# Performance work log

Hardware: AMD Instinct MI355X
Metric: run time of the kernel (lower is better)

## Reference

```python
import jax, jax.numpy as jnp
import numpy as np

N_NODES = 50000
N_EDGES = 800000
D_IN = 128
D_OUT = 128


def setup_inputs() -> dict:
    key = jax.random.key(0)
    k1, k2, k3, k4, k5 = jax.random.split(key, 5)
    x = jax.random.normal(k1, (N_NODES, D_IN), dtype=jnp.float32)
    edge_index = jax.random.randint(k2, (2, N_EDGES), 0, N_NODES, dtype=jnp.int64)
    scale = 1.0 / np.sqrt(D_IN)
    W_rel = jax.random.normal(k3, (D_OUT, D_IN), dtype=jnp.float32) * scale
    b_rel = jax.random.normal(k4, (D_OUT,), dtype=jnp.float32) * scale
    W_root = jax.random.normal(k5, (D_OUT, D_IN), dtype=jnp.float32) * scale
    return {"x": x, "edge_index": edge_index, "W_rel": W_rel, "b_rel": b_rel, "W_root": W_root}


def reference(x, edge_index, W_rel, b_rel, W_root):
    # PyG GraphConv (aggr='add'):
    #   out_i = W_rel @ (sum_{j->i} x_j) + b_rel + W_root @ x_i
    # followed by ReLU (normalization=None, dropout=0 -> identity).
    src = edge_index[0]  # message source j
    dst = edge_index[1]  # message target i
    n = x.shape[0]
    agg = jax.ops.segment_sum(x[src], dst, num_segments=n)  # [N, D_IN]
    out = agg @ W_rel.T + b_rel + x @ W_root.T              # [N, D_OUT]
    return jax.nn.relu(out)
```

## Files before the change

kernel.cpp:

```cpp
#include <hip/hip_runtime.h>
#include <hip/hip_bf16.h>


#define N_NODES 50000
#define N_EDGES 800000
#define D 128
#define SLOTS 40
#define NB 782
#define BCAP 1536
#define BINB 196
#define NPB 32
#define KC 32
#define SROW 136

#define CVT_N  (N_NODES * (D / 2))
#define PACK_N (8 * 8 * 64 * 8)

typedef __attribute__((ext_vector_type(8))) short short8;
typedef __attribute__((ext_vector_type(4))) float floatx4;

__device__ __forceinline__ float bf2f(unsigned short u) {
    return __uint_as_float((unsigned int)u << 16);
}
__device__ __forceinline__ unsigned short f2bf(float f) {
    __hip_bfloat16 h = __float2bfloat16(f);
    return *(unsigned short*)&h;
}

__device__ __forceinline__ int wave_detect_i64(const int* __restrict__ ei) {
    int lane = threadIdx.x & 63;
    int v = ei[2 * lane + 1];
    return __ballot(v == 0) == ~0ull;
}

__global__ __launch_bounds__(256) void zero_f4_kernel(float4* __restrict__ p, int n4) {
    int i = blockIdx.x * 256 + threadIdx.x;
    if (i < n4) p[i] = make_float4(0.f, 0.f, 0.f, 0.f);
}

__global__ void detect_kernel(const int* __restrict__ ei, int* __restrict__ flag) {
    if (threadIdx.x == 0 && blockIdx.x == 0) {
        int any = 0;
        for (int i = 0; i < 64; ++i) any |= ei[2 * i + 1];
        flag[0] = (any == 0) ? 1 : 0;
    }
}

__global__ __launch_bounds__(256) void stage1_kernel(const float2* __restrict__ x2,
                                                     ushort2* __restrict__ xb2,
                                                     const float* __restrict__ Wrel,
                                                     const float* __restrict__ Wroot,
                                                     unsigned short* __restrict__ pwc,
                                                     const int* __restrict__ ei,
                                                     int* __restrict__ gcur,
                                                     unsigned* __restrict__ bmem,
                                                     int* __restrict__ ovf_cnt,
                                                     int* __restrict__ ovf) {
    __shared__ int lds_cnt[NB];
    __shared__ int lds_base[NB];
    if (blockIdx.x < BINB) {
        int t = threadIdx.x;
        int i64 = wave_detect_i64(ei);
        for (int i = t; i < NB; i += 256) lds_cnt[i] = 0;
        __syncthreads();

        unsigned rec[16];
        int rnk[16];
#pragma unroll
        for (int g = 0; g < 4; ++g) {
            int base = blockIdx.x * 4096 + g * 1024 + t * 4;
            int s0 = -1, s1 = -1, s2 = -1, s3 = -1;
            int d0 = -1, d1 = -1, d2 = -1, d3 = -1;
            if (base < N_EDGES) {
                if (i64) {
                    int4 a = *(const int4*)&ei[2 * base];
                    int4 b = *(const int4*)&ei[2 * base + 4];
                    s0 = a.x; s1 = a.z; s2 = b.x; s3 = b.z;
                    int4 c = *(const int4*)&ei[2 * N_EDGES + 2 * base];
                    int4 e = *(const int4*)&ei[2 * N_EDGES + 2 * base + 4];
                    d0 = c.x; d1 = c.z; d2 = e.x; d3 = e.z;
                } else {
                    int4 sv = *(const int4*)&ei[base];
                    int4 dv = *(const int4*)&ei[N_EDGES + base];
                    s0 = sv.x; s1 = sv.y; s2 = sv.z; s3 = sv.w;
                    d0 = dv.x; d1 = dv.y; d2 = dv.z; d3 = dv.w;
                }
            }
#define BINP(idx, ss, dd)                                                        \
            {                                                                    \
                bool ok = (unsigned)(ss) < N_NODES && (unsigned)(dd) < N_NODES;  \
                rec[idx] = ok ? (((unsigned)(dd) << 16) | (unsigned)(ss))        \
                              : 0xFFFFFFFFu;                                     \
                rnk[idx] = ok ? atomicAdd(&lds_cnt[(unsigned)(dd) >> 6], 1) : 0; \
            }
            BINP(g * 4 + 0, s0, d0)
            BINP(g * 4 + 1, s1, d1)
            BINP(g * 4 + 2, s2, d2)
            BINP(g * 4 + 3, s3, d3)
#undef BINP
        }
        __syncthreads();
        for (int i = t; i < NB; i += 256) {
            int c = lds_cnt[i];
            lds_base[i] = c ? atomicAdd(&gcur[i], c) : 0;
        }
        __syncthreads();
#pragma unroll
        for (int idx = 0; idx < 16; ++idx) {
            unsigned r = rec[idx];
            if (r != 0xFFFFFFFFu) {
                int bk = (int)(r >> 22);
                int pos = lds_base[bk] + rnk[idx];
                if (pos < BCAP) {
                    bmem[(size_t)bk * BCAP + pos] = r;
                } else {
                    int o = atomicAdd(ovf_cnt, 1);
                    ovf[2 * o] = (int)(r >> 16);
                    ovf[2 * o + 1] = (int)(r & 0xFFFFu);
                }
            }
        }
    } else {
        int i = (blockIdx.x - BINB) * 256 + threadIdx.x;
        if (i < CVT_N) {
            float2 f = x2[i];
            xb2[i] = make_ushort2(f2bf(f.x), f2bf(f.y));
        } else if (i < CVT_N + PACK_N) {
            int idx  = i - CVT_N;
            int j    = idx & 7;
            int lane = (idx >> 3) & 63;
            int n0   = (idx >> 9) & 7;
            int t    = idx >> 12;
            int n = n0 * 16 + (lane & 15);
            int k = t * 32 + (lane >> 4) * 8 + j;
            float w = (k < D) ? Wrel[n * D + k] : Wroot[n * D + (k - D)];
            pwc[idx] = f2bf(w);
        }
    }
}

__global__ __launch_bounds__(256) void GraphConvLayer_55783035240593_kernel(
        const ushort2* __restrict__ xb2,
        const unsigned short* __restrict__ xb,
        const int* __restrict__ gcur,
        const unsigned* __restrict__ bmem,
        const int* __restrict__ ovf_cnt,
        const int* __restrict__ ovf,
        const unsigned short* __restrict__ pwc,
        const float* __restrict__ b_rel,
        float* __restrict__ out) {
    __shared__ unsigned short sA[32 * SROW];
    __shared__ unsigned short slotsL[32 * SLOTS];
    __shared__ int lc[32];
    int t = threadIdx.x;
    int wid = t >> 6, lane = t & 63;
    int bkt = blockIdx.x >> 1, half = blockIdx.x & 1;
    int node0 = blockIdx.x * 32;

    if (t < 32) lc[t] = 0;
    __syncthreads();

    int n = gcur[bkt];
    if (n > BCAP) n = BCAP;
    for (int e = t; e < n; e += 256) {
        unsigned r = bmem[(size_t)bkt * BCAP + e];
        int d = (int)(r >> 16);
        if (((d >> 5) & 1) != half) continue;
        int p = atomicAdd(&lc[d & 31], 1);
        if (p < SLOTS) slotsL[(d & 31) * SLOTS + p] = (unsigned short)(r & 0xFFFFu);
    }
    __syncthreads();
    int tov = ovf_cnt[0];

    for (int pp = 0; pp < 4; ++pp) {
        int la = wid * 8 + pp * 2, lb = la + 1;
        int nodeA = node0 + la, nodeB = node0 + lb;
        int kkA = lc[la], kkB = lc[lb];
        int kA = (kkA > SLOTS) ? 0 : kkA;
        int kB = (kkB > SLOTS) ? 0 : kkB;
        int myA = (lane < kA) ? (int)slotsL[la * SLOTS + lane] : 0;
        int myB = (lane < kB) ? (int)slotsL[lb * SLOTS + lane] : 0;
        float axA = 0.f, ayA = 0.f, axB = 0.f, ayB = 0.f;
        int jmax = kA > kB ? kA : kB;
        for (int j = 0; j < jmax; j += 8) {
            bool doA = j < kA, doB = j < kB;
            ushort2 u[8], v[8];
            if (doA) {
                int s[8];
#pragma unroll
                for (int i = 0; i < 8; ++i) s[i] = __shfl(myA, j + i);
#pragma unroll
                for (int i = 0; i < 8; ++i) u[i] = xb2[(size_t)s[i] * (D / 2) + lane];
            }
            if (doB) {
                int s[8];
#pragma unroll
                for (int i = 0; i < 8; ++i) s[i] = __shfl(myB, j + i);
#pragma unroll
                for (int i = 0; i < 8; ++i) v[i] = xb2[(size_t)s[i] * (D / 2) + lane];
            }
            if (doA) {
#pragma unroll
                for (int i = 0; i < 8; ++i) {
                    float mm = (j + i < kA) ? 1.f : 0.f;
                    axA += mm * bf2f(u[i].x);
                    ayA += mm * bf2f(u[i].y);
                }
            }
            if (doB) {
#pragma unroll
                for (int i = 0; i < 8; ++i) {
                    float mm = (j + i < kB) ? 1.f : 0.f;
                    axB += mm * bf2f(v[i].x);
                    ayB += mm * bf2f(v[i].y);
                }
            }
        }
        if (kkA > SLOTS) {
            for (int e = 0; e < n; ++e) {
                unsigned r = bmem[(size_t)bkt * BCAP + e];
                if ((int)(r >> 16) == nodeA) {
                    ushort2 uu = xb2[(size_t)(r & 0xFFFFu) * (D / 2) + lane];
                    axA += bf2f(uu.x); ayA += bf2f(uu.y);
                }
            }
        }
        if (kkB > SLOTS) {
            for (int e = 0; e < n; ++e) {
                unsigned r = bmem[(size_t)bkt * BCAP + e];
                if ((int)(r >> 16) == nodeB) {
                    ushort2 uu = xb2[(size_t)(r & 0xFFFFu) * (D / 2) + lane];
                    axB += bf2f(uu.x); ayB += bf2f(uu.y);
                }
            }
        }
        if (tov > 0) {
            for (int e2 = 0; e2 < tov; ++e2) {
                int dd = ovf[2 * e2];
                if (dd == nodeA) {
                    ushort2 uu = xb2[(size_t)ovf[2 * e2 + 1] * (D / 2) + lane];
                    axA += bf2f(uu.x); ayA += bf2f(uu.y);
                } else if (dd == nodeB) {
                    ushort2 uu = xb2[(size_t)ovf[2 * e2 + 1] * (D / 2) + lane];
                    axB += bf2f(uu.x); ayB += bf2f(uu.y);
                }
            }
        }
        *(ushort2*)&sA[la * SROW + 2 * lane] = make_ushort2(f2bf(axA), f2bf(ayA));
        *(ushort2*)&sA[lb * SROW + 2 * lane] = make_ushort2(f2bf(axB), f2bf(ayB));
    }
    __syncthreads();

    int m = lane & 15, quad = lane >> 4;
    int tl = wid >> 1, ng0 = (wid & 1) * 4;
    const unsigned short* arow = &sA[(tl * 16 + m) * SROW + quad * 8];
    int xnode = node0 + tl * 16 + m;
    if (xnode >= N_NODES) xnode = 0;
    const unsigned short* xrow = xb + (size_t)xnode * D + quad * 8;

    floatx4 acc0 = (floatx4){0.f, 0.f, 0.f, 0.f};
    floatx4 acc1 = (floatx4){0.f, 0.f, 0.f, 0.f};
    floatx4 acc2 = (floatx4){0.f, 0.f, 0.f, 0.f};
    floatx4 acc3 = (floatx4){0.f, 0.f, 0.f, 0.f};
#pragma unroll
    for (int tt = 0; tt < 8; ++tt) {
        short8 afrag = (tt < 4) ? *(const short8*)(arow + tt * 32)
                                : *(const short8*)(xrow + (tt - 4) * 32);
        const unsigned short* bb = pwc + ((size_t)(tt * 8 + ng0) * 64 + lane) * 8;
        short8 b0 = *(const short8*)bb;
        short8 b1 = *(const short8*)(bb + 1 * 64 * 8);
        short8 b2 = *(const short8*)(bb + 2 * 64 * 8);
        short8 b3 = *(const short8*)(bb + 3 * 64 * 8);
        acc0 = __builtin_amdgcn_mfma_f32_16x16x32_bf16(afrag, b0, acc0, 0, 0, 0);
        acc1 = __builtin_amdgcn_mfma_f32_16x16x32_bf16(afrag, b1, acc1, 0, 0, 0);
        acc2 = __builtin_amdgcn_mfma_f32_16x16x32_bf16(afrag, b2, acc2, 0, 0, 0);
        acc3 = __builtin_amdgcn_mfma_f32_16x16x32_bf16(afrag, b3, acc3, 0, 0, 0);
    }

#pragma unroll
    for (int q = 0; q < 4; ++q) {
        floatx4 a = (q == 0) ? acc0 : (q == 1) ? acc1 : (q == 2) ? acc2 : acc3;
        int nn = (ng0 + q) * 16 + m;
        float bias = b_rel[nn];
#pragma unroll
        for (int r = 0; r < 4; ++r) {
            int node = node0 + tl * 16 + quad * 4 + r;
            if (node < N_NODES)
                out[(size_t)node * D + nn] = fmaxf(a[r] + bias, 0.f);
        }
    }
}

__global__ __launch_bounds__(256) void pack_w_kernel(const float* __restrict__ W,
                                                     float* __restrict__ pw) {
    int idx = blockIdx.x * 256 + threadIdx.x;
    if (idx >= D * D) return;
    int o = idx >> 7, k = idx & 127;
    pw[k * D + o] = W[o * D + k];
}

__global__ __launch_bounds__(256) void hist_kernel(const int* __restrict__ ei,
                                                   int* __restrict__ deg) {
    int i64 = wave_detect_i64(ei);
    int base = (blockIdx.x * 256 + threadIdx.x) * 4;
    if (base >= N_EDGES) return;
    int d0, d1, d2, d3;
    if (i64) {
        int4 a = *(const int4*)&ei[2 * N_EDGES + 2 * base];
        int4 b = *(const int4*)&ei[2 * N_EDGES + 2 * base + 4];
        d0 = a.x; d1 = a.z; d2 = b.x; d3 = b.z;
    } else {
        int4 v = *(const int4*)&ei[N_EDGES + base];
        d0 = v.x; d1 = v.y; d2 = v.z; d3 = v.w;
    }
    if ((unsigned)d0 < N_NODES) atomicAdd(&deg[d0], 1);
    if ((unsigned)d1 < N_NODES) atomicAdd(&deg[d1], 1);
    if ((unsigned)d2 < N_NODES) atomicAdd(&deg[d2], 1);
    if ((unsigned)d3 < N_NODES) atomicAdd(&deg[d3], 1);
}

__device__ __forceinline__ int wave_iscan(int v, int lane) {
#pragma unroll
    for (int off = 1; off < 64; off <<= 1) {
        int u = __shfl_up(v, off, 64);
        if (lane >= off) v += u;
    }
    return v;
}

__global__ __launch_bounds__(1024) void scan_kernel(const int* __restrict__ deg,
                                                    int* __restrict__ offsets,
                                                    int* __restrict__ cursor) {
    __shared__ int wsum[16];
    __shared__ int base_s;
    int t = threadIdx.x, lane = t & 63, w = t >> 6;
    if (t == 0) { base_s = 0; offsets[0] = 0; }
    __syncthreads();
    for (int c0 = 0; c0 < N_NODES; c0 += 1024) {
        int idx = c0 + t;
        int v = (idx < N_NODES) ? deg[idx] : 0;
        int inc = wave_iscan(v, lane);
        if (lane == 63) wsum[w] = inc;
        __syncthreads();
        if (w == 0) {
            int s = (lane < 16) ? wsum[lane] : 0;
            int si = wave_iscan(s, lane);
            if (lane < 16) wsum[lane] = si - s;
        }
        __syncthreads();
        int tot = base_s + wsum[w] + inc;
        if (idx < N_NODES) {
            offsets[idx + 1] = tot;
            cursor[idx] = tot - v;
        }
        __syncthreads();
        if (t == 1023) base_s = tot;
        __syncthreads();
    }
}

__global__ __launch_bounds__(256) void reorder_kernel(const int* __restrict__ ei,
                                                      int* __restrict__ cursor,
                                                      int* __restrict__ csr_src) {
    int i64 = wave_detect_i64(ei);
    int base = (blockIdx.x * 256 + threadIdx.x) * 4;
    if (base >= N_EDGES) return;
    int s0, s1, s2, s3, d0, d1, d2, d3;
    if (i64) {
        int4 a = *(const int4*)&ei[2 * base];
        int4 b = *(const int4*)&ei[2 * base + 4];
        s0 = a.x; s1 = a.z; s2 = b.x; s3 = b.z;
        int4 c = *(const int4*)&ei[2 * N_EDGES + 2 * base];
        int4 e = *(const int4*)&ei[2 * N_EDGES + 2 * base + 4];
        d0 = c.x; d1 = c.z; d2 = e.x; d3 = e.z;
    } else {
        int4 sv = *(const int4*)&ei[base];
        int4 dv = *(const int4*)&ei[N_EDGES + base];
        s0 = sv.x; s1 = sv.y; s2 = sv.z; s3 = sv.w;
        d0 = dv.x; d1 = dv.y; d2 = dv.z; d3 = dv.w;
    }
    bool v0 = (unsigned)s0 < N_NODES && (unsigned)d0 < N_NODES;
    bool v1 = (unsigned)s1 < N_NODES && (unsigned)d1 < N_NODES;
    bool v2 = (unsigned)s2 < N_NODES && (unsigned)d2 < N_NODES;
    bool v3 = (unsigned)s3 < N_NODES && (unsigned)d3 < N_NODES;
    int p0 = v0 ? atomicAdd(&cursor[d0], 1) : 0;
    int p1 = v1 ? atomicAdd(&cursor[d1], 1) : 0;
    int p2 = v2 ? atomicAdd(&cursor[d2], 1) : 0;
    int p3 = v3 ? atomicAdd(&cursor[d3], 1) : 0;
    if (v0) csr_src[p0] = s0;
    if (v1) csr_src[p1] = s1;
    if (v2) csr_src[p2] = s2;
    if (v3) csr_src[p3] = s3;
}

__global__ __launch_bounds__(256) void gather_kernel(const float2* __restrict__ x2,
                                                     const int* __restrict__ csr_src,
                                                     const int* __restrict__ offsets,
                                                     float2* __restrict__ agg2) {
    int node = blockIdx.x * 4 + (threadIdx.x >> 6);
    int lane = threadIdx.x & 63;
    if (node >= N_NODES) return;
    int beg = offsets[node], end = offsets[node + 1];
    float2 acc = make_float2(0.f, 0.f);
    for (int e = beg; e < end; ++e) {
        int s = csr_src[e];
        float2 f = x2[(size_t)s * (D / 2) + lane];
        acc.x += f.x;
        acc.y += f.y;
    }
    agg2[(size_t)node * (D / 2) + lane] = acc;
}

__global__ __launch_bounds__(256) void scatter_kernel(const float2* __restrict__ x2,
                                                      const int* __restrict__ ei,
                                                      const int* __restrict__ flag,
                                                      float* __restrict__ agg) {
    int wave = threadIdx.x >> 6;
    int lane = threadIdx.x & 63;
    int e = blockIdx.x * 4 + wave;
    if (e >= N_EDGES) return;
    int i64 = flag ? flag[0] : 0;
    int s, d;
    if (i64) { s = ei[2 * e]; d = ei[2 * N_EDGES + 2 * e]; }
    else     { s = ei[e];     d = ei[N_EDGES + e]; }
    if ((unsigned)s >= N_NODES || (unsigned)d >= N_NODES) return;
    float2 f = x2[(size_t)s * (D / 2) + lane];
    atomicAdd(&agg[(size_t)d * D + 2 * lane + 0], f.x);
    atomicAdd(&agg[(size_t)d * D + 2 * lane + 1], f.y);
}

__global__ __launch_bounds__(256) void gemm_f32_kernel(
        const float2* __restrict__ x2,
        const float* __restrict__ pwrel,
        const float* __restrict__ pwroot,
        const float* __restrict__ b_rel,
        float* __restrict__ out) {
    __shared__ float sWrel[KC * D];
    __shared__ float sWroot[KC * D];
    __shared__ float2 sAm[NPB * (KC / 2)];
    __shared__ float2 sXm[NPB * (KC / 2)];

    int t = threadIdx.x;
    int node0 = blockIdx.x * NPB;
    int tn = t >> 5;
    int to = t & 31;

    float acc[4][4];
#pragma unroll
    for (int a = 0; a < 4; ++a)
#pragma unroll
        for (int b = 0; b < 4; ++b) acc[a][b] = 0.0f;

    for (int c = 0; c < 4; ++c) {
        __syncthreads();
#pragma unroll
        for (int r = 0; r < 4; ++r) {
            int i = r * 256 + t;
            ((float4*)sWrel)[i]  = ((const float4*)(pwrel  + c * KC * D))[i];
            ((float4*)sWroot)[i] = ((const float4*)(pwroot + c * KC * D))[i];
        }
#pragma unroll
        for (int r = 0; r < 2; ++r) {
            int i = r * 256 + t;
            int n = i >> 4, k2 = i & 15;
            int node = node0 + n;
            float2 av = make_float2(0.f, 0.f), xv = make_float2(0.f, 0.f);
            if (node < N_NODES) {
                av = ((const float2*)out)[(size_t)node * (D / 2) + c * (KC / 2) + k2];
                xv = x2[(size_t)node * (D / 2) + c * (KC / 2) + k2];
            }
            sAm[i] = av;
            sXm[i] = xv;
        }
        __syncthreads();

#pragma unroll
        for (int k2 = 0; k2 < KC / 2; ++k2) {
            float4 wr0 = *(const float4*)&sWrel[(2 * k2 + 0) * D + to * 4];
            float4 wr1 = *(const float4*)&sWrel[(2 * k2 + 1) * D + to * 4];
            float4 wt0 = *(const float4*)&sWroot[(2 * k2 + 0) * D + to * 4];
            float4 wt1 = *(const float4*)&sWroot[(2 * k2 + 1) * D + to * 4];
#pragma unroll
            for (int ni = 0; ni < 4; ++ni) {
                float2 a  = sAm[(tn * 4 + ni) * (KC / 2) + k2];
                float2 xx = sXm[(tn * 4 + ni) * (KC / 2) + k2];
                acc[ni][0] += a.x * wr0.x + a.y * wr1.x + xx.x * wt0.x + xx.y * wt1.x;
                acc[ni][1] += a.x * wr0.y + a.y * wr1.y + xx.x * wt0.y + xx.y * wt1.y;
                acc[ni][2] += a.x * wr0.z + a.y * wr1.z + xx.x * wt0.z + xx.y * wt1.z;
                acc[ni][3] += a.x * wr0.w + a.y * wr1.w + xx.x * wt0.w + xx.y * wt1.w;
            }
        }
    }

    int o0 = to * 4;
    float4 bias = *(const float4*)&b_rel[o0];
#pragma unroll
    for (int ni = 0; ni < 4; ++ni) {
        int node = node0 + tn * 4 + ni;
        if (node >= N_NODES) continue;
        float4 v;
        v.x = fmaxf(acc[ni][0] + bias.x, 0.f);
        v.y = fmaxf(acc[ni][1] + bias.y, 0.f);
        v.z = fmaxf(acc[ni][2] + bias.z, 0.f);
        v.w = fmaxf(acc[ni][3] + bias.w, 0.f);
        *(float4*)&out[(size_t)node * D + o0] = v;
    }
}

__global__ __launch_bounds__(128) void gemm_fallback_kernel(const float* __restrict__ x,
                                                            const float* __restrict__ Wrel,
                                                            const float* __restrict__ Wroot,
                                                            const float* __restrict__ b_rel,
                                                            float* __restrict__ out) {
    __shared__ float rowA[D];
    __shared__ float rowX[D];
    int node = blockIdx.x;
    int o = threadIdx.x;
    rowA[o] = out[(size_t)node * D + o];
    rowX[o] = x[(size_t)node * D + o];
    __syncthreads();
    float acc = b_rel[o];
    const float4* wr = (const float4*)&Wrel[o * D];
    const float4* wt = (const float4*)&Wroot[o * D];
#pragma unroll 8
    for (int k4 = 0; k4 < D / 4; ++k4) {
        float4 w = wr[k4], u = wt[k4];
        const float* a = &rowA[k4 * 4];
        const float* xx = &rowX[k4 * 4];
        acc += a[0] * w.x + a[1] * w.y + a[2] * w.z + a[3] * w.w
             + xx[0] * u.x + xx[1] * u.y + xx[2] * u.z + xx[3] * u.w;
    }
    __syncthreads();
    out[(size_t)node * D + o] = fmaxf(acc, 0.f);
}

extern "C" void kernel_launch(void* const* d_in, const int* in_sizes, int n_in,
                              void* d_out, int out_size, void* d_ws, size_t ws_size,
                              hipStream_t stream) {
    const float* x      = (const float*)d_in[0];
    const int*   ei     = (const int*)d_in[1];
    const float* W_rel  = (const float*)d_in[2];
    const float* b_rel  = (const float*)d_in[3];
    const float* W_root = (const float*)d_in[4];
    float*       out    = (float*)d_out;

    char* p = (char*)d_ws;
    size_t o0 = 16;
    int*            flag    = (int*)p;
    unsigned short* pwc     = (unsigned short*)(p + o0);  o0 += (size_t)PACK_N * 2;
    unsigned short* xb      = (unsigned short*)(p + o0);  o0 += (size_t)N_NODES * D * 2;
    const size_t gcur_pad = ((size_t)NB * 4 + 15) & ~(size_t)15;
    int*            gcur    = (int*)(p + o0);             o0 += gcur_pad;
    int*            ovf_cnt = (int*)(p + o0);             o0 += 16;
    unsigned*       bmem    = (unsigned*)(p + o0);        o0 += (size_t)NB * BCAP * 4;
    int*            ovf     = (int*)(p + o0);             o0 += (size_t)N_EDGES * 8;
    const size_t need_full = o0;

    size_t m0 = 16;
    float* m_pwrel  = (float*)(p + m0);  m0 += (size_t)D * D * 4;
    float* m_pwroot = (float*)(p + m0);  m0 += (size_t)D * D * 4;
    int*   m_deg    = (int*)(p + m0);    m0 += (size_t)N_NODES * 4;
    int*   m_offs   = (int*)(p + m0);    m0 += ((size_t)N_NODES + 1) * 4 + 12;
    m0 &= ~15ull;
    int*   m_csr    = (int*)(p + m0);    m0 += (size_t)N_EDGES * 4;
    const size_t need_mid = m0;
    const size_t need_pw  = 16 + 2 * (size_t)D * D * 4;

    const int eb4 = (N_EDGES / 4 + 255) / 256;

    if (ws_size >= need_full) {
        hipMemsetAsync(gcur, 0, gcur_pad + 16, stream);
        const int prep_total = CVT_N + PACK_N;
        const int grid1 = BINB + (prep_total + 255) / 256;
        stage1_kernel<<<grid1, 256, 0, stream>>>(
            (const float2*)x, (ushort2*)xb, W_rel, W_root, pwc, ei,
            gcur, bmem, ovf_cnt, ovf);
        GraphConvLayer_55783035240593_kernel<<<2 * NB, 256, 0, stream>>>(
            (const ushort2*)xb, xb, gcur, bmem, ovf_cnt, ovf, pwc, b_rel, out);
    } else if (ws_size >= need_mid) {
        pack_w_kernel<<<64, 256, 0, stream>>>(W_rel, m_pwrel);
        pack_w_kernel<<<64, 256, 0, stream>>>(W_root, m_pwroot);
        zero_f4_kernel<<<(N_NODES / 4 + 255) / 256, 256, 0, stream>>>((float4*)m_deg,
                                                                      N_NODES / 4);
        hist_kernel<<<eb4, 256, 0, stream>>>(ei, m_deg);
        scan_kernel<<<1, 1024, 0, stream>>>(m_deg, m_offs, m_deg);
        reorder_kernel<<<eb4, 256, 0, stream>>>(ei, m_deg, m_csr);
        gather_kernel<<<N_NODES / 4, 256, 0, stream>>>((const float2*)x, m_csr,
                                                       m_offs, (float2*)out);
        gemm_f32_kernel<<<(N_NODES + NPB - 1) / NPB, 256, 0, stream>>>(
            (const float2*)x, m_pwrel, m_pwroot, b_rel, out);
    } else {
        bool have_flag = ws_size >= 16;
        bool have_pw   = ws_size >= need_pw;
        if (have_flag) detect_kernel<<<1, 64, 0, stream>>>(ei, flag);
        if (have_pw) {
            pack_w_kernel<<<64, 256, 0, stream>>>(W_rel, m_pwrel);
            pack_w_kernel<<<64, 256, 0, stream>>>(W_root, m_pwroot);
        }
        int n4 = N_NODES * D / 4;
        zero_f4_kernel<<<(n4 + 255) / 256, 256, 0, stream>>>((float4*)out, n4);
        scatter_kernel<<<N_EDGES / 4, 256, 0, stream>>>((const float2*)x, ei,
                                                        have_flag ? flag : nullptr, out);
        if (have_pw)
            gemm_f32_kernel<<<(N_NODES + NPB - 1) / NPB, 256, 0, stream>>>(
                (const float2*)x, m_pwrel, m_pwroot, b_rel, out);
        else
            gemm_fallback_kernel<<<N_NODES, 128, 0, stream>>>(x, W_rel, W_root, b_rel, out);
    }
}
```

Measured before the change: 151.6 us.

## Shrink node buckets to 16 nodes per block, removing half-bucket filtering

Edges are now binned into buckets of 16 destination nodes (3125 buckets, capacity 384) instead of 64-node buckets, so each main-kernel block owns one whole bucket and no longer scans and discards the other half's records. The block tile drops from 32 to 16 nodes, and each wave now computes two 16-column MFMA output tiles instead of four. The binning kernel reuses the count array for bucket bases to save LDS. The trade-offs are more global atomics on the bucket cursors, smaller MFMA work per block with less weight reuse, and a higher chance of bucket overflow landing in the slow overflow path.

```diff
diff --git a/kernel.cpp b/kernel.cpp
--- a/kernel.cpp
+++ b/kernel.cpp
@@ -5,9 +5,9 @@
 #define N_NODES 50000
 #define N_EDGES 800000
 #define D 128
-#define SLOTS 40
-#define NB 782
-#define BCAP 1536
+#define SLOTS 48
+#define NB 3125
+#define BCAP 384
 #define BINB 196
 #define NPB 32
 #define KC 32
@@ -57,7 +57,6 @@
                                                      int* __restrict__ ovf_cnt,
                                                      int* __restrict__ ovf) {
     __shared__ int lds_cnt[NB];
-    __shared__ int lds_base[NB];
     if (blockIdx.x < BINB) {
         int t = threadIdx.x;
         int i64 = wave_detect_i64(ei);
@@ -91,7 +90,7 @@
                 bool ok = (unsigned)(ss) < N_NODES && (unsigned)(dd) < N_NODES;  \
                 rec[idx] = ok ? (((unsigned)(dd) << 16) | (unsigned)(ss))        \
                               : 0xFFFFFFFFu;                                     \
-                rnk[idx] = ok ? atomicAdd(&lds_cnt[(unsigned)(dd) >> 6], 1) : 0; \
+                rnk[idx] = ok ? atomicAdd(&lds_cnt[(unsigned)(dd) >> 4], 1) : 0; \
             }
             BINP(g * 4 + 0, s0, d0)
             BINP(g * 4 + 1, s1, d1)
@@ -102,15 +101,16 @@
         __syncthreads();
         for (int i = t; i < NB; i += 256) {
             int c = lds_cnt[i];
-            lds_base[i] = c ? atomicAdd(&gcur[i], c) : 0;
+            int b = c ? atomicAdd(&gcur[i], c) : 0;
+            lds_cnt[i] = b;
         }
         __syncthreads();
 #pragma unroll
         for (int idx = 0; idx < 16; ++idx) {
             unsigned r = rec[idx];
             if (r != 0xFFFFFFFFu) {
-                int bk = (int)(r >> 22);
-                int pos = lds_base[bk] + rnk[idx];
+                int bk = (int)(r >> 20);
+                int pos = lds_cnt[bk] + rnk[idx];
                 if (pos < BCAP) {
                     bmem[(size_t)bk * BCAP + pos] = r;
                 } else {
@@ -149,31 +149,30 @@
         const unsigned short* __restrict__ pwc,
         const float* __restrict__ b_rel,
         float* __restrict__ out) {
-    __shared__ unsigned short sA[32 * SROW];
-    __shared__ unsigned short slotsL[32 * SLOTS];
-    __shared__ int lc[32];
+    __shared__ unsigned short sA[16 * SROW];
+    __shared__ unsigned short slotsL[16 * SLOTS];
+    __shared__ int lc[16];
     int t = threadIdx.x;
     int wid = t >> 6, lane = t & 63;
-    int bkt = blockIdx.x >> 1, half = blockIdx.x & 1;
-    int node0 = blockIdx.x * 32;
-
-    if (t < 32) lc[t] = 0;
+    int bkt = blockIdx.x;
+    int node0 = bkt * 16;
+
+    int n = gcur[bkt];
+    int tov = ovf_cnt[0];
+    if (t < 16) lc[t] = 0;
     __syncthreads();
 
-    int n = gcur[bkt];
     if (n > BCAP) n = BCAP;
     for (int e = t; e < n; e += 256) {
         unsigned r = bmem[(size_t)bkt * BCAP + e];
-        int d = (int)(r >> 16);
-        if (((d >> 5) & 1) != half) continue;
-        int p = atomicAdd(&lc[d & 31], 1);
-        if (p < SLOTS) slotsL[(d & 31) * SLOTS + p] = (unsigned short)(r & 0xFFFFu);
+        int dl = (int)((r >> 16) & 15);
+        int p = atomicAdd(&lc[dl], 1);
+        if (p < SLOTS) slotsL[dl * SLOTS + p] = (unsigned short)(r & 0xFFFFu);
     }
     __syncthreads();
-    int tov = ovf_cnt[0];
-
-    for (int pp = 0; pp < 4; ++pp) {
-        int la = wid * 8 + pp * 2, lb = la + 1;
+
+    for (int pp = 0; pp < 2; ++pp) {
+        int la = wid * 4 + pp * 2, lb = la + 1;
         int nodeA = node0 + la, nodeB = node0 + lb;
         int kkA = lc[la], kkB = lc[lb];
         int kA = (kkA > SLOTS) ? 0 : kkA;
@@ -252,41 +251,31 @@
     __syncthreads();
 
     int m = lane & 15, quad = lane >> 4;
-    int tl = wid >> 1, ng0 = (wid & 1) * 4;
-    const unsigned short* arow = &sA[(tl * 16 + m) * SROW + quad * 8];
-    int xnode = node0 + tl * 16 + m;
-    if (xnode >= N_NODES) xnode = 0;
-    const unsigned short* xrow = xb + (size_t)xnode * D + quad * 8;
+    const unsigned short* arow = &sA[m * SROW + quad * 8];
+    const unsigned short* xrow = xb + (size_t)(node0 + m) * D + quad * 8;
 
     floatx4 acc0 = (floatx4){0.f, 0.f, 0.f, 0.f};
     floatx4 acc1 = (floatx4){0.f, 0.f, 0.f, 0.f};
-    floatx4 acc2 = (floatx4){0.f, 0.f, 0.f, 0.f};
-    floatx4 acc3 = (floatx4){0.f, 0.f, 0.f, 0.f};
 #pragma unroll
     for (int tt = 0; tt < 8; ++tt) {
         short8 afrag = (tt < 4) ? *(const short8*)(arow + tt * 32)
                                 : *(const short8*)(xrow + (tt - 4) * 32);
-        const unsigned short* bb = pwc + ((size_t)(tt * 8 + ng0) * 64 + lane) * 8;
+        const unsigned short* bb = pwc + ((size_t)(tt * 8 + wid * 2) * 64 + lane) * 8;
         short8 b0 = *(const short8*)bb;
-        short8 b1 = *(const short8*)(bb + 1 * 64 * 8);
-        short8 b2 = *(const short8*)(bb + 2 * 64 * 8);
-        short8 b3 = *(const short8*)(bb + 3 * 64 * 8);
+        short8 b1 = *(const short8*)(bb + 64 * 8);
         acc0 = __builtin_amdgcn_mfma_f32_16x16x32_bf16(afrag, b0, acc0, 0, 0, 0);
         acc1 = __builtin_amdgcn_mfma_f32_16x16x32_bf16(afrag, b1, acc1, 0, 0, 0);
-        acc2 = __builtin_amdgcn_mfma_f32_16x16x32_bf16(afrag, b2, acc2, 0, 0, 0);
-        acc3 = __builtin_amdgcn_mfma_f32_16x16x32_bf16(afrag, b3, acc3, 0, 0, 0);
-    }
-
-#pragma unroll
-    for (int q = 0; q < 4; ++q) {
-        floatx4 a = (q == 0) ? acc0 : (q == 1) ? acc1 : (q == 2) ? acc2 : acc3;
-        int nn = (ng0 + q) * 16 + m;
+    }
+
+#pragma unroll
+    for (int q = 0; q < 2; ++q) {
+        floatx4 a = q ? acc1 : acc0;
+        int nn = (wid * 2 + q) * 16 + m;
         float bias = b_rel[nn];
 #pragma unroll
         for (int r = 0; r < 4; ++r) {
-            int node = node0 + tl * 16 + quad * 4 + r;
-            if (node < N_NODES)
-                out[(size_t)node * D + nn] = fmaxf(a[r] + bias, 0.f);
+            int node = node0 + quad * 4 + r;
+            out[(size_t)node * D + nn] = fmaxf(a[r] + bias, 0.f);
         }
     }
 }
@@ -575,7 +564,7 @@
         stage1_kernel<<<grid1, 256, 0, stream>>>(
             (const float2*)x, (ushort2*)xb, W_rel, W_root, pwc, ei,
             gcur, bmem, ovf_cnt, ovf);
-        GraphConvLayer_55783035240593_kernel<<<2 * NB, 256, 0, stream>>>(
+        GraphConvLayer_55783035240593_kernel<<<NB, 256, 0, stream>>>(
             (const ushort2*)xb, xb, gcur, bmem, ovf_cnt, ovf, pwc, b_rel, out);
     } else if (ws_size >= need_mid) {
         pack_w_kernel<<<64, 256, 0, stream>>>(W_rel, m_pwrel);
```

Result: no change. 149.5 us (-1.4%).
